# Kernel optimization log

Measured on AMD Instinct MI355X. Metric: run time of the kernel, lower is better.

## Reference

```python
import jax, jax.numpy as jnp
import numpy as np

B, T, D = 256, 512, 8      # batch, seq_len, Feature_number
H = 120                    # hidden_size
L = 4                      # layers=['s','s','s','s']
NH = D                     # num_heads = Feature_number
HD = H // NH               # head dim = 15
EPS = 1e-5


def setup_inputs() -> dict:
    key = jax.random.key(0)
    ks = jax.random.split(key, 16)
    rn = lambda k, shape, s=0.1: (jax.random.normal(k, shape, jnp.float32) * s)
    return {
        "x":   jax.random.normal(ks[0], (B, T, D), jnp.float32),
        # input->gate weights, stacked over layers
        "Wi":  rn(ks[1], (L, H, D)),
        "Wf":  rn(ks[2], (L, H, D)),
        "Wz":  rn(ks[3], (L, H, D)),
        "Wo":  rn(ks[4], (L, H, D)),
        # block-diagonal (multi-head) recurrent weights: [L, NH, HD, HD]
        "Ri":  rn(ks[5], (L, NH, HD, HD)),
        "Rf":  rn(ks[6], (L, NH, HD, HD)),
        "Rz":  rn(ks[7], (L, NH, HD, HD)),
        "Ro":  rn(ks[8], (L, NH, HD, HD)),
        "bi":  rn(ks[9],  (L, H), 0.02),
        "bf":  rn(ks[10], (L, H), 0.02),
        "bz":  rn(ks[11], (L, H), 0.02),
        "bo":  rn(ks[12], (L, H), 0.02),
        # per-block down-projection back to Feature_number (residual block)
        "Wp":  rn(ks[13], (L, D, H)),
        "bp":  jnp.zeros((L, D), jnp.float32),
        # BatchNorm1d(Feature_number) affine params
        "gamma": jnp.ones((D,), jnp.float32),
        "beta":  jnp.zeros((D,), jnp.float32),
        # fc5: Linear(Feature_number, 1)
        "Wfc": rn(ks[14], (1, D)),
        "bfc": jnp.zeros((1,), jnp.float32),
    }


def _slstm_layer(x, Wi, Wf, Wz, Wo, Ri, Rf, Rz, Ro, bi, bf, bz, bo, Wp, bp):
    """One sLSTM block: exp-gated recurrence with stabilizer, then down-proj + residual.
    x: [B, T, D] -> [B, T, D]."""
    Bn = x.shape[0]

    def rec(h, R):  # block-diagonal recurrent matmul: [B,H] x [NH,HD,HD] -> [B,H]
        return jnp.einsum("bnd,nde->bne", h.reshape(Bn, NH, HD), R).reshape(Bn, H)

    def step(carry, x_t):
        h, c, n, m = carry                       # each [B, H]
        it = x_t @ Wi.T + rec(h, Ri) + bi        # input gate pre-act
        ft = x_t @ Wf.T + rec(h, Rf) + bf        # forget gate pre-act (exp gating)
        z = jnp.tanh(x_t @ Wz.T + rec(h, Rz) + bz)
        o = jax.nn.sigmoid(x_t @ Wo.T + rec(h, Ro) + bo)
        m_new = jnp.maximum(ft + m, it)          # stabilizer state
        i_p = jnp.exp(it - m_new)
        f_p = jnp.exp(ft + m - m_new)
        c_new = f_p * c + i_p * z
        n_new = f_p * n + i_p                    # normalizer state
        h_new = o * (c_new / n_new)
        return (h_new, c_new, n_new, m_new), h_new

    z0 = jnp.zeros((Bn, H), x.dtype)
    (_, _, _, _), hs = jax.lax.scan(step, (z0, z0, z0, z0), jnp.swapaxes(x, 0, 1))
    y = jnp.einsum("tbh,dh->tbd", hs, Wp) + bp   # down-project to D
    return x + jnp.swapaxes(y, 0, 1)             # residual


def reference(x, Wi, Wf, Wz, Wo, Ri, Rf, Rz, Ro, bi, bf, bz, bo, Wp, bp,
              gamma, beta, Wfc, bfc):
    h = x
    for l in range(L):
        h = _slstm_layer(h, Wi[l], Wf[l], Wz[l], Wo[l], Ri[l], Rf[l], Rz[l], Ro[l],
                         bi[l], bf[l], bz[l], bo[l], Wp[l], bp[l])
    last = h[:, -1, :]                            # [B, D]
    # BatchNorm1d in training mode (batch stats, biased variance)
    mu = jnp.mean(last, axis=0)
    var = jnp.mean((last - mu) ** 2, axis=0)
    bn = (last - mu) / jnp.sqrt(var + EPS) * gamma + beta
    out = jax.nn.sigmoid(bn @ Wfc.T + bfc)        # [B, 1]
    return out[:, 0]                              # squeeze(1) -> [B]
```

## Files before the change

### kernel.cpp

```cpp
#include <hip/hip_runtime.h>
#include <math.h>

#define Bsz 256
#define T   512
#define Dd  8
#define Hh  120
#define Ll  4
#define NHn 8
#define HDd 15
#define HP  16
#define EPSf 1e-5f

__device__ __forceinline__ float fast_rcp(float x) {
#if __has_builtin(__builtin_amdgcn_rcpf)
    return __builtin_amdgcn_rcpf(x);
#else
    return 1.f / x;
#endif
}
__device__ __forceinline__ float tanh_fast(float x) {
    float e = __expf(2.f * x);
    return 1.f - 2.f * fast_rcp(e + 1.f);
}
__device__ __forceinline__ float sigm_fast(float x) {
    return fast_rcp(1.f + __expf(-x));
}

__global__ __launch_bounds__(512, 2) void slstm_kernel(
    const float* __restrict__ x,
    const float* __restrict__ Wi, const float* __restrict__ Wf,
    const float* __restrict__ Wz, const float* __restrict__ Wo,
    const float* __restrict__ Ri, const float* __restrict__ Rf,
    const float* __restrict__ Rz, const float* __restrict__ Ro,
    const float* __restrict__ bi, const float* __restrict__ bf,
    const float* __restrict__ bz, const float* __restrict__ bo,
    const float* __restrict__ Wp, const float* __restrict__ bp,
    float* __restrict__ last_out)
{
    __shared__ __align__(16) float xs[T * Dd];
    __shared__ __align__(16) float hb[Ll][2][NHn * HP];

    const int tid = threadIdx.x;
    const int b   = blockIdx.x;
    const int l   = tid >> 7;
    const int j   = tid & 127;

    {
        const float4* xg  = (const float4*)(x + (size_t)b * T * Dd);
        float4*       xs4 = (float4*)xs;
        xs4[tid]       = xg[tid];
        xs4[tid + 512] = xg[tid + 512];
        ((float*)hb)[tid]       = 0.f;
        ((float*)hb)[tid + 512] = 0.f;
    }

    const bool gl = (j < Hh);
    int n = 0;
    float wI[Dd], wF[Dd], wZ[Dd], wO[Dd];
    float rI[HDd], rF[HDd], rZ[HDd], rO[HDd];
    float bI = 0.f, bF = 0.f, bZ = 0.f, bO = 0.f;
    if (gl) {
        n = j / HDd;
        const int e   = j - n * HDd;
        const int row = (l * Hh + j) * Dd;
#pragma unroll
        for (int d = 0; d < Dd; ++d) {
            wI[d] = Wi[row + d]; wF[d] = Wf[row + d];
            wZ[d] = Wz[row + d]; wO[d] = Wo[row + d];
        }
        const int rb = ((l * NHn + n) * HDd) * HDd + e;
#pragma unroll
        for (int d = 0; d < HDd; ++d) {
            rI[d] = Ri[rb + d * HDd]; rF[d] = Rf[rb + d * HDd];
            rZ[d] = Rz[rb + d * HDd]; rO[d] = Ro[rb + d * HDd];
        }
        bI = bi[l * Hh + j]; bF = bf[l * Hh + j];
        bZ = bz[l * Hh + j]; bO = bo[l * Hh + j];
    }

    const int d8 = j & 7, ch = j >> 3;
    float wp_r[HDd];
    float bp_r = 0.f;
    if (j < 64) {
        const int base = l * Dd * Hh + d8 * Hh + ch * HDd;
#pragma unroll
        for (int k = 0; k < HDd; ++k) wp_r[k] = Wp[base + k];
        if (j < Dd) bp_r = bp[l * Dd + j];
    }

    float cst = 0.f, nst = 0.f, mst = 0.f;

    __syncthreads();

    for (int tau = 0; tau < T + Ll - 1; ++tau) {
        const int t   = tau - l;
        const bool act = (t >= 0) && (t < T);

        if (act && gl) {
            const float4* xt4 = (const float4*)(xs + t * Dd);
            const float4 xa = xt4[0], xb2 = xt4[1];
            const float xv[Dd] = {xa.x, xa.y, xa.z, xa.w, xb2.x, xb2.y, xb2.z, xb2.w};
            float gi = bI, gf = bF, gz = bZ, go = bO;
#pragma unroll
            for (int d = 0; d < Dd; ++d) {
                gi = fmaf(xv[d], wI[d], gi);
                gf = fmaf(xv[d], wF[d], gf);
                gz = fmaf(xv[d], wZ[d], gz);
                go = fmaf(xv[d], wO[d], go);
            }
            const float4* h4 = (const float4*)(&hb[l][t & 1][n * HP]);
            const float4 h0 = h4[0], h1 = h4[1], h2 = h4[2], h3 = h4[3];
            const float hv[16] = {h0.x, h0.y, h0.z, h0.w, h1.x, h1.y, h1.z, h1.w,
                                  h2.x, h2.y, h2.z, h2.w, h3.x, h3.y, h3.z, h3.w};
#pragma unroll
            for (int d = 0; d < HDd; ++d) {
                gi = fmaf(hv[d], rI[d], gi);
                gf = fmaf(hv[d], rF[d], gf);
                gz = fmaf(hv[d], rZ[d], gz);
                go = fmaf(hv[d], rO[d], go);
            }
            const float z  = tanh_fast(gz);
            const float o  = sigm_fast(go);
            const float mn = fmaxf(gf + mst, gi);
            const float ip = __expf(gi - mn);
            const float fp = __expf(gf + mst - mn);
            cst = fmaf(fp, cst, ip * z);
            nst = fmaf(fp, nst, ip);
            mst = mn;
            const float hnew = o * cst * fast_rcp(nst);
            hb[l][(t & 1) ^ 1][n * HP + (j - n * HDd)] = hnew;
        }
        __syncthreads();

        if (act && (j < 64)) {
            const float* hn = &hb[l][(t & 1) ^ 1][ch * HP];
            float s = 0.f;
#pragma unroll
            for (int k = 0; k < HDd; ++k) s = fmaf(hn[k], wp_r[k], s);
            s += __shfl_xor(s, 8);
            s += __shfl_xor(s, 16);
            s += __shfl_xor(s, 32);
            if (j < Dd) xs[t * Dd + j] += s + bp_r;
        }
        __syncthreads();
    }

    if (tid < Dd) last_out[b * Dd + tid] = xs[(T - 1) * Dd + tid];
}

__global__ __launch_bounds__(Bsz) void bn_fc_kernel(
    const float* __restrict__ last,
    const float* __restrict__ gamma, const float* __restrict__ beta,
    const float* __restrict__ Wfc,   const float* __restrict__ bfc,
    float* __restrict__ out)
{
    __shared__ float ls[Bsz][Dd];
    __shared__ float mu[Dd], rstdg[Dd], bet[Dd], wfc[Dd];
    const int tid = threadIdx.x;
#pragma unroll
    for (int d = 0; d < Dd; ++d) ls[tid][d] = last[tid * Dd + d];
    __syncthreads();
    if (tid < Dd) {
        float s = 0.f;
        for (int bb = 0; bb < Bsz; ++bb) s += ls[bb][tid];
        const float mean = s * (1.f / Bsz);
        float v = 0.f;
        for (int bb = 0; bb < Bsz; ++bb) {
            const float dd = ls[bb][tid] - mean;
            v += dd * dd;
        }
        v *= (1.f / Bsz);
        mu[tid]    = mean;
        rstdg[tid] = rsqrtf(v + EPSf) * gamma[tid];
        bet[tid]   = beta[tid];
        wfc[tid]   = Wfc[tid];
    }
    __syncthreads();
    float acc = bfc[0];
#pragma unroll
    for (int d = 0; d < Dd; ++d)
        acc += ((ls[tid][d] - mu[d]) * rstdg[d] + bet[d]) * wfc[d];
    out[tid] = sigm_fast(acc);
}

extern "C" void kernel_launch(void* const* d_in, const int* in_sizes, int n_in,
                              void* d_out, int out_size, void* d_ws, size_t ws_size,
                              hipStream_t stream) {
    const float* x    = (const float*)d_in[0];
    const float* Wi   = (const float*)d_in[1];
    const float* Wf   = (const float*)d_in[2];
    const float* Wz   = (const float*)d_in[3];
    const float* Wo   = (const float*)d_in[4];
    const float* Ri   = (const float*)d_in[5];
    const float* Rf   = (const float*)d_in[6];
    const float* Rz   = (const float*)d_in[7];
    const float* Ro   = (const float*)d_in[8];
    const float* bi   = (const float*)d_in[9];
    const float* bf   = (const float*)d_in[10];
    const float* bz   = (const float*)d_in[11];
    const float* bo   = (const float*)d_in[12];
    const float* Wp   = (const float*)d_in[13];
    const float* bp   = (const float*)d_in[14];
    const float* gamma= (const float*)d_in[15];
    const float* beta = (const float*)d_in[16];
    const float* Wfc  = (const float*)d_in[17];
    const float* bfc  = (const float*)d_in[18];

    float* last_ws = (float*)d_ws;
    float* out     = (float*)d_out;

    slstm_kernel<<<Bsz, 512, 0, stream>>>(x, Wi, Wf, Wz, Wo, Ri, Rf, Rz, Ro,
                                          bi, bf, bz, bo, Wp, bp, last_ws);
    bn_fc_kernel<<<1, Bsz, 0, stream>>>(last_ws, gamma, beta, Wfc, bfc, out);
}
```

Before: 468.0 us.

## Skew layer pipeline to remove one barrier per timestep and overlap down-projection

Layers are now offset by two timesteps instead of one. The down-projection for step t-1 runs in the otherwise idle lanes 64..127 during the same phase as the gate computation for step t, which removes the second __syncthreads per iteration. Parameter loads become unconditional, and empty asm statements pin the weights in VGPRs. This adds a few pipeline fill steps and extra register pressure, and it relies on the double-buffered h reads not racing with writes under a single barrier.

```diff
diff --git a/kernel.cpp b/kernel.cpp
--- a/kernel.cpp
+++ b/kernel.cpp
@@ -55,14 +55,13 @@
     }
 
     const bool gl = (j < Hh);
-    int n = 0;
+    const int jj  = gl ? j : 0;
+    const int n   = jj / HDd;
+    const int e   = jj - n * HDd;
     float wI[Dd], wF[Dd], wZ[Dd], wO[Dd];
     float rI[HDd], rF[HDd], rZ[HDd], rO[HDd];
-    float bI = 0.f, bF = 0.f, bZ = 0.f, bO = 0.f;
-    if (gl) {
-        n = j / HDd;
-        const int e   = j - n * HDd;
-        const int row = (l * Hh + j) * Dd;
+    {
+        const int row = (l * Hh + jj) * Dd;
 #pragma unroll
         for (int d = 0; d < Dd; ++d) {
             wI[d] = Wi[row + d]; wF[d] = Wf[row + d];
@@ -74,30 +73,43 @@
             rI[d] = Ri[rb + d * HDd]; rF[d] = Rf[rb + d * HDd];
             rZ[d] = Rz[rb + d * HDd]; rO[d] = Ro[rb + d * HDd];
         }
-        bI = bi[l * Hh + j]; bF = bf[l * Hh + j];
-        bZ = bz[l * Hh + j]; bO = bo[l * Hh + j];
-    }
-
-    const int d8 = j & 7, ch = j >> 3;
-    float wp_r[HDd];
-    float bp_r = 0.f;
-    if (j < 64) {
+    }
+    float bI = bi[l * Hh + jj], bF = bf[l * Hh + jj];
+    float bZ = bz[l * Hh + jj], bO = bo[l * Hh + jj];
+
+    const int p  = (j >= 64) ? (j - 64) : j;
+    const int d8 = p & 7, ch = p >> 3;
+    float wp_r[16];
+    {
         const int base = l * Dd * Hh + d8 * Hh + ch * HDd;
 #pragma unroll
         for (int k = 0; k < HDd; ++k) wp_r[k] = Wp[base + k];
-        if (j < Dd) bp_r = bp[l * Dd + j];
-    }
+        wp_r[15] = 0.f;
+    }
+    float bp_r = bp[l * Dd + d8];
+
+#pragma unroll
+    for (int d = 0; d < Dd; ++d)
+        asm volatile("" : "+v"(wI[d]), "+v"(wF[d]), "+v"(wZ[d]), "+v"(wO[d]));
+#pragma unroll
+    for (int d = 0; d < HDd; ++d)
+        asm volatile("" : "+v"(rI[d]), "+v"(rF[d]), "+v"(rZ[d]), "+v"(rO[d]));
+#pragma unroll
+    for (int k = 0; k < 16; ++k)
+        asm volatile("" : "+v"(wp_r[k]));
+    asm volatile("" : "+v"(bI), "+v"(bF), "+v"(bZ), "+v"(bO));
+    asm volatile("" : "+v"(bp_r));
 
     float cst = 0.f, nst = 0.f, mst = 0.f;
 
     __syncthreads();
 
-    for (int tau = 0; tau < T + Ll - 1; ++tau) {
-        const int t   = tau - l;
-        const bool act = (t >= 0) && (t < T);
-
-        if (act && gl) {
-            const float4* xt4 = (const float4*)(xs + t * Dd);
+    for (int tau = 0; tau < T + 2 * Ll - 1; ++tau) {
+        const int t_g = tau - 2 * l;
+        const int t_p = t_g - 1;
+
+        if (gl && (t_g >= 0) && (t_g < T)) {
+            const float4* xt4 = (const float4*)(xs + t_g * Dd);
             const float4 xa = xt4[0], xb2 = xt4[1];
             const float xv[Dd] = {xa.x, xa.y, xa.z, xa.w, xb2.x, xb2.y, xb2.z, xb2.w};
             float gi = bI, gf = bF, gz = bZ, go = bO;
@@ -108,7 +120,7 @@
                 gz = fmaf(xv[d], wZ[d], gz);
                 go = fmaf(xv[d], wO[d], go);
             }
-            const float4* h4 = (const float4*)(&hb[l][t & 1][n * HP]);
+            const float4* h4 = (const float4*)(&hb[l][t_g & 1][n * HP]);
             const float4 h0 = h4[0], h1 = h4[1], h2 = h4[2], h3 = h4[3];
             const float hv[16] = {h0.x, h0.y, h0.z, h0.w, h1.x, h1.y, h1.z, h1.w,
                                   h2.x, h2.y, h2.z, h2.w, h3.x, h3.y, h3.z, h3.w};
@@ -128,20 +140,23 @@
             nst = fmaf(fp, nst, ip);
             mst = mn;
             const float hnew = o * cst * fast_rcp(nst);
-            hb[l][(t & 1) ^ 1][n * HP + (j - n * HDd)] = hnew;
-        }
-        __syncthreads();
-
-        if (act && (j < 64)) {
-            const float* hn = &hb[l][(t & 1) ^ 1][ch * HP];
+            hb[l][(t_g & 1) ^ 1][n * HP + e] = hnew;
+        }
+
+        if ((j >= 64) && (t_p >= 0) && (t_p < T)) {
+            const float4* h4 = (const float4*)(&hb[l][t_g & 1][ch * HP]);
+            const float4 h0 = h4[0], h1 = h4[1], h2 = h4[2], h3 = h4[3];
+            const float hv[16] = {h0.x, h0.y, h0.z, h0.w, h1.x, h1.y, h1.z, h1.w,
+                                  h2.x, h2.y, h2.z, h2.w, h3.x, h3.y, h3.z, h3.w};
             float s = 0.f;
 #pragma unroll
-            for (int k = 0; k < HDd; ++k) s = fmaf(hn[k], wp_r[k], s);
+            for (int k = 0; k < 16; ++k) s = fmaf(hv[k], wp_r[k], s);
             s += __shfl_xor(s, 8);
             s += __shfl_xor(s, 16);
             s += __shfl_xor(s, 32);
-            if (j < Dd) xs[t * Dd + j] += s + bp_r;
-        }
+            if (p < Dd) xs[t_p * Dd + p] += s + bp_r;
+        }
+
         __syncthreads();
     }
 
```

New measurement: 453.1 us. 1.03x faster.
